# Kernel optimization log

Hardware: AMD Instinct MI355X
Metric: run time of the kernel (lower is better)

Reference implementation:

```python
import jax, jax.numpy as jnp
import numpy as np


def _gru_layer(x, w_ih, w_hh, b_ih, b_hh):
    # x: (T, B, I); w_ih: (3H, I); w_hh: (3H, H). PyTorch gate order: r, z, n.
    H = w_hh.shape[1]
    xg = jnp.einsum('tbi,gi->tbg', x, w_ih) + b_ih  # precompute input gates (T, B, 3H)

    def step(h, xg_t):
        hg = h @ w_hh.T + b_hh
        xr, xz, xn = jnp.split(xg_t, 3, axis=-1)
        hr, hz, hn = jnp.split(hg, 3, axis=-1)
        r = jax.nn.sigmoid(xr + hr)
        z = jax.nn.sigmoid(xz + hz)
        n = jnp.tanh(xn + r * hn)
        h_new = (1.0 - z) * n + z * h
        return h_new, h_new

    h0 = jnp.zeros((x.shape[1], H), dtype=x.dtype)
    _, out = jax.lax.scan(step, h0, xg)
    return out  # (T, B, H)


def setup_inputs() -> dict:
    key = jax.random.key(0)
    ks = jax.random.split(key, 16)
    T, B, V, E, H1, H2 = 1024, 128, 128, 312, 256, 128

    def u(k, shape, fan):
        s = 1.0 / np.sqrt(fan)
        return jax.random.uniform(k, shape, jnp.float32, -s, s)

    return {
        'token': jax.random.randint(ks[0], (T, B), 0, V),
        'emb': jax.random.normal(ks[1], (V, E), jnp.float32),
        'w_ih1': u(ks[2], (3 * H1, E), H1),
        'w_hh1': u(ks[3], (3 * H1, H1), H1),
        'b_ih1': u(ks[4], (3 * H1,), H1),
        'b_hh1': u(ks[5], (3 * H1,), H1),
        'ln_g': jnp.ones((H1,), jnp.float32),
        'ln_b': jnp.zeros((H1,), jnp.float32),
        'w_ih2f': u(ks[6], (3 * H2, H1), H2),
        'w_hh2f': u(ks[7], (3 * H2, H2), H2),
        'b_ih2f': u(ks[8], (3 * H2,), H2),
        'b_hh2f': u(ks[9], (3 * H2,), H2),
        'w_ih2b': u(ks[10], (3 * H2, H1), H2),
        'w_hh2b': u(ks[11], (3 * H2, H2), H2),
        'b_ih2b': u(ks[12], (3 * H2,), H2),
        'b_hh2b': u(ks[13], (3 * H2,), H2),
    }


def reference(token, emb, w_ih1, w_hh1, b_ih1, b_hh1, ln_g, ln_b,
              w_ih2f, w_hh2f, b_ih2f, b_hh2f, w_ih2b, w_hh2b, b_ih2b, b_hh2b):
    LN_EPS = 256.0  # torch.nn.LayerNorm(256, 256): second positional arg is eps (faithful)
    x = emb[token]                                        # (T, B, 312)
    h = _gru_layer(x, w_ih1, w_hh1, b_ih1, b_hh1)         # (T, B, 256)
    mu = jnp.mean(h, axis=-1, keepdims=True)
    var = jnp.mean((h - mu) ** 2, axis=-1, keepdims=True)
    hn = (h - mu) / jnp.sqrt(var + LN_EPS) * ln_g + ln_b  # LayerNorm over last dim
    fwd = _gru_layer(hn, w_ih2f, w_hh2f, b_ih2f, b_hh2f)                 # (T, B, 128)
    bwd = _gru_layer(hn[::-1], w_ih2b, w_hh2b, b_ih2b, b_hh2b)[::-1]     # (T, B, 128)
    return jnp.concatenate([fwd, bwd], axis=-1)           # (T, B, 256)
```

## Files before the change

### kernel.cpp

```cpp
#include <hip/hip_runtime.h>
#include <hip/hip_bf16.h>
#include <stdint.h>

typedef __attribute__((ext_vector_type(8))) short short8;
typedef __attribute__((ext_vector_type(4))) float f32x4;
typedef unsigned long long u64;
typedef unsigned int u32;

__device__ __forceinline__ float bf2f(unsigned short s){
  union { float f; u32 u; } v; v.u = ((u32)s) << 16; return v.f;
}
__device__ __forceinline__ unsigned short f2bf(float f){
  u32 u = __float_as_uint(f);
  u32 r = (u + 0x7fffu + ((u >> 16) & 1u)) >> 16;
  return (unsigned short)r;
}
__device__ __forceinline__ float sigm(float x){ return 1.0f / (1.0f + __expf(-x)); }
__device__ __forceinline__ float tanh_(float x){ return 1.0f - 2.0f/(__expf(2.0f*x) + 1.0f); }
__device__ __forceinline__ u64 pack4(float a, float b, float c, float d){
  return (u64)f2bf(a) | ((u64)f2bf(b)<<16) | ((u64)f2bf(c)<<32) | ((u64)f2bf(d)<<48);
}
__device__ __forceinline__ void gl_lds16(const void* g, void* l){
  __builtin_amdgcn_global_load_lds(
      (const __attribute__((address_space(1))) unsigned int*)g,
      (__attribute__((address_space(3))) unsigned int*)l, 16, 0, 0);
}

__global__ void k_pack(const float* __restrict__ w_hh1,
                       const float* __restrict__ w_ih2f, const float* __restrict__ w_ih2b,
                       const float* __restrict__ w_hh2f, const float* __restrict__ w_hh2b,
                       unsigned short* __restrict__ pack1,
                       unsigned short* __restrict__ pack2,
                       unsigned short* __restrict__ pack3)
{
  int tid = blockIdx.x*256 + threadIdx.x;
  const float* src;
  unsigned short* dst;
  long idx;
  if (tid < 24576){
    int f = tid>>6, l = tid&63;
    int w = f/48, rem = f%48, m = rem>>3, kt = rem&7;
    int g  = ((m>>1)<<8) + (w<<5) + ((m&1)<<4) + (l&15);
    int kb = (kt<<5) + ((l>>4)<<3);
    src = w_hh1 + (size_t)g*256 + kb;
    dst = pack1; idx = tid;
  } else if (tid < 49152){
    int t2 = tid - 24576;
    int f = t2>>6, l = t2&63;
    int w = f/48, rem = f%48, m = rem>>3, kt = rem&7;
    int G  = 96*w + (m<<4) + (l&15);
    int kb = (kt<<5) + ((l>>4)<<3);
    const float* W = (G < 384) ? w_ih2f : w_ih2b;
    src = W + (size_t)(G % 384)*256 + kb;
    dst = pack2; idx = t2;
  } else {
    int t3 = tid - 49152;
    int f = t3>>6, l = t3&63;
    int dir = f/96, r96 = f%96, w = r96/12, r12 = r96%12, m = r12>>2, kt = r12&3;
    int Grow = (m<<7) + (w<<4) + (l&15);
    int kb = (kt<<5) + ((l>>4)<<3);
    src = (dir ? w_hh2b : w_hh2f) + (size_t)Grow*128 + kb;
    dst = pack3; idx = t3;
  }
  u64 lo = (u64)f2bf(src[0]) | ((u64)f2bf(src[1])<<16) | ((u64)f2bf(src[2])<<32) | ((u64)f2bf(src[3])<<48);
  u64 hi = (u64)f2bf(src[4]) | ((u64)f2bf(src[5])<<16) | ((u64)f2bf(src[6])<<32) | ((u64)f2bf(src[7])<<48);
  *(u64*)(dst + (size_t)idx*8)     = lo;
  *(u64*)(dst + (size_t)idx*8 + 4) = hi;
}

__global__ void k_xgv(const float* __restrict__ emb, const float* __restrict__ w_ih1,
                      const float* __restrict__ b_ih1, const float* __restrict__ b_hh1,
                      float* __restrict__ xgV)
{
  int tid = blockIdx.x*256 + threadIdx.x;
  int v = tid / 768, g = tid % 768;
  float s = b_ih1[g] + (g < 512 ? b_hh1[g] : 0.0f);
  const f32x4* e4 = (const f32x4*)(emb   + (size_t)v*312);
  const f32x4* w4 = (const f32x4*)(w_ih1 + (size_t)g*312);
  #pragma unroll 4
  for (int i=0;i<78;i++){
    f32x4 a = e4[i], b = w4[i];
    s += a[0]*b[0] + a[1]*b[1] + a[2]*b[2] + a[3]*b[3];
  }
  xgV[tid] = s;
}

__launch_bounds__(512)
__global__ void k_scan1(const int* __restrict__ token,
                        const float* __restrict__ xgV,
                        const unsigned short* __restrict__ pack1,
                        const float* __restrict__ b_hh1,
                        const float* __restrict__ ln_g, const float* __restrict__ ln_b,
                        unsigned short* __restrict__ hn)
{
  __shared__ __align__(16) char hb[2][8192];
  __shared__ __align__(16) char xgb[2][49152];
  __shared__ __align__(16) float lngb[512];
  __shared__ __align__(16) float bnl[256];
  __shared__ __align__(8)  float2 scr[2][8][16];

  const int tid = threadIdx.x;
  const int w = tid>>6, lane = tid&63, hi = lane>>4, col = lane&15;
  const int b0 = blockIdx.x * 16;

  short8 wf[6][8];
  #pragma unroll
  for (int m=0;m<6;m++)
    #pragma unroll
    for (int kt=0;kt<8;kt++)
      wf[m][kt] = *(const short8*)(pack1 + (size_t)((((w*6+m)<<3)+kt)*64 + lane)*8);

  if (tid < 256) lngb[tid] = ln_g[tid]; else lngb[tid] = ln_b[tid-256];
  if (tid < 256) bnl[tid] = b_hh1[512 + tid];
  for (int i = tid; i < 2048; i += 512) ((u32*)hb[0])[i] = 0;
  f32x4 hr[2]; hr[0] = (f32x4){0,0,0,0}; hr[1] = (f32x4){0,0,0,0};

  auto stage = [&](int tt, int buf){
    int tok = token[tt*128 + b0 + (tid & 15)];
    const char* src = (const char*)xgV + (size_t)tok*3072 + ((tid>>4)<<4);
    char* dst = xgb[buf] + tid*16;
    #pragma unroll
    for (int k=0;k<6;k++)
      gl_lds16(src + k*512, dst + k*8192);
  };
  stage(0, 0);
  __syncthreads();

  for (int t=0; t<1024; t++){
    const int cur = t & 1, nxt = cur ^ 1;
    if (t < 1023) stage(t+1, nxt);

    f32x4 acc[6];
    #pragma unroll
    for (int m=0;m<6;m++) acc[m] = (f32x4){0,0,0,0};
    #pragma unroll
    for (int kt=0;kt<8;kt++){
      short8 hf = *(const short8*)(hb[cur] + ((kt<<2)+hi)*256 + (col<<4));
      #pragma unroll
      for (int m=0;m<6;m++)
        acc[m] = __builtin_amdgcn_mfma_f32_16x16x32_bf16(wf[m][kt], hf, acc[m], 0, 0, 0);
    }

    float s1 = 0.f, s2 = 0.f;
    #pragma unroll
    for (int nt=0;nt<2;nt++){
      const int ub = (w<<5) + (nt<<4) + (hi<<2);
      const char* xb = xgb[cur] + (col<<4);
      f32x4 xr = *(const f32x4*)(xb + (size_t)ub*64);
      f32x4 xz = *(const f32x4*)(xb + (size_t)(256+ub)*64);
      f32x4 xn = *(const f32x4*)(xb + (size_t)(512+ub)*64);
      f32x4 bn4 = *(const f32x4*)(bnl + ub);
      #pragma unroll
      for (int j=0;j<4;j++){
        float r  = sigm(xr[j] + acc[nt][j]);
        float z  = sigm(xz[j] + acc[2+nt][j]);
        float nn = tanh_(xn[j] + r*(acc[4+nt][j] + bn4[j]));
        float h  = nn + z*(hr[nt][j] - nn);
        hr[nt][j] = h;
        s1 += h; s2 += h*h;
      }
      u64 pk = pack4(hr[nt][0], hr[nt][1], hr[nt][2], hr[nt][3]);
      *(u64*)(hb[nxt] + (ub>>3)*256 + (col<<4) + ((hi&1)<<3)) = pk;
    }
    s1 += __shfl_xor(s1, 16); s1 += __shfl_xor(s1, 32);
    s2 += __shfl_xor(s2, 16); s2 += __shfl_xor(s2, 32);
    if (hi == 0){ scr[cur][w][col] = make_float2(s1, s2); }
    __syncthreads();

    float S1 = 0.f, S2 = 0.f;
    #pragma unroll
    for (int ww=0; ww<8; ww++){ float2 v = scr[cur][ww][col]; S1 += v.x; S2 += v.y; }
    float mu  = S1 * (1.0f/256.0f);
    float var = S2 * (1.0f/256.0f) - mu*mu;
    float rs  = rsqrtf(var + 256.0f);
    #pragma unroll
    for (int nt=0;nt<2;nt++){
      const int ub = (w<<5) + (nt<<4) + (hi<<2);
      f32x4 g4 = *(const f32x4*)&lngb[ub];
      f32x4 e4 = *(const f32x4*)&lngb[256+ub];
      u64 pk = pack4((hr[nt][0]-mu)*rs*g4[0] + e4[0],
                     (hr[nt][1]-mu)*rs*g4[1] + e4[1],
                     (hr[nt][2]-mu)*rs*g4[2] + e4[2],
                     (hr[nt][3]-mu)*rs*g4[3] + e4[3]);
      *(u64*)(hn + (size_t)(t*128 + b0 + col)*256 + ub) = pk;
    }
  }
}

__launch_bounds__(512)
__global__ void k_k3(const unsigned short* __restrict__ hn,
                     const unsigned short* __restrict__ pack2,
                     unsigned short* __restrict__ xg2f,
                     unsigned short* __restrict__ xg2b)
{
  const int tid = threadIdx.x;
  const int w = tid>>6, lane = tid&63, hi = lane>>4, col = lane&15;
  short8 wf[6][8];
  #pragma unroll
  for (int m=0;m<6;m++)
    #pragma unroll
    for (int kt=0;kt<8;kt++)
      wf[m][kt] = *(const short8*)(pack2 + (size_t)((((w*6+m)<<3)+kt)*64 + lane)*8);
  const int dir = w >> 2;
  unsigned short* dst = dir ? xg2b : xg2f;

  for (int it=0; it<16; it++){
    int tb0 = blockIdx.x*256 + it*16;
    const unsigned short* hrow = hn + (size_t)(tb0 + col)*256;
    f32x4 acc[6];
    #pragma unroll
    for (int m=0;m<6;m++) acc[m] = (f32x4){0,0,0,0};
    #pragma unroll
    for (int h2=0; h2<2; h2++){
      short8 bf[4];
      #pragma unroll
      for (int i=0;i<4;i++) bf[i] = *(const short8*)(hrow + (((h2<<2)+i)<<5) + (hi<<3));
      #pragma unroll
      for (int i=0;i<4;i++)
        #pragma unroll
        for (int m=0;m<6;m++)
          acc[m] = __builtin_amdgcn_mfma_f32_16x16x32_bf16(wf[m][(h2<<2)+i], bf[i], acc[m], 0, 0, 0);
    }
    #pragma unroll
    for (int m=0;m<6;m++){
      int Gl = 96*w + (m<<4) + (hi<<2) - dir*384;
      u64 pk = pack4(acc[m][0], acc[m][1], acc[m][2], acc[m][3]);
      *(u64*)(dst + (size_t)(tb0 + col)*384 + Gl) = pk;
    }
  }
}

__launch_bounds__(512)
__global__ void k_scan2(const unsigned short* __restrict__ xg2f,
                        const unsigned short* __restrict__ xg2b,
                        const unsigned short* __restrict__ pack3,
                        const float* __restrict__ b_ih2f, const float* __restrict__ b_hh2f,
                        const float* __restrict__ b_ih2b, const float* __restrict__ b_hh2b,
                        float* __restrict__ out)
{
  __shared__ __align__(16) char hb[2][4096];
  const int tid = threadIdx.x;
  const int w = tid>>6, lane = tid&63, hi = lane>>4, col = lane&15;
  const int blk = blockIdx.x;
  const int dir = blk >> 3;
  const int b0  = (blk & 7) * 16;
  const unsigned short* xg = dir ? xg2b : xg2f;
  const float* bi = dir ? b_ih2b : b_ih2f;
  const float* bh = dir ? b_hh2b : b_hh2f;

  short8 wf[3][4];
  #pragma unroll
  for (int m=0;m<3;m++)
    #pragma unroll
    for (int kt=0;kt<4;kt++)
      wf[m][kt] = *(const short8*)(pack3 + (size_t)(((dir*96 + w*12 + (m<<2) + kt))*64 + lane)*8);

  const int u = (w<<4) + (hi<<2);
  f32x4 bir = *(const f32x4*)(bi + u),        bhr = *(const f32x4*)(bh + u);
  f32x4 biz = *(const f32x4*)(bi + 128 + u),  bhz = *(const f32x4*)(bh + 128 + u);
  f32x4 bin = *(const f32x4*)(bi + 256 + u),  bhn = *(const f32x4*)(bh + 256 + u);
  f32x4 bcr = bir + bhr, bcz = biz + bhz;

  for (int i = tid; i < 1024; i += 512) ((u32*)hb[0])[i] = 0;
  f32x4 hcur = (f32x4){0,0,0,0};

  int te0 = dir ? 1023 : 0;
  const unsigned short* p0 = xg + (size_t)(te0*128 + b0 + col)*384;
  u64 xr_n = *(const u64*)(p0 + u);
  u64 xz_n = *(const u64*)(p0 + 128 + u);
  u64 xn_n = *(const u64*)(p0 + 256 + u);
  __syncthreads();

  for (int t=0; t<1024; t++){
    const int cur = t & 1, nxt = cur ^ 1;
    u64 xr = xr_n, xz = xz_n, xn = xn_n;
    if (t < 1023){
      int te1 = dir ? (1022 - t) : (t + 1);
      const unsigned short* p = xg + (size_t)(te1*128 + b0 + col)*384;
      xr_n = *(const u64*)(p + u);
      xz_n = *(const u64*)(p + 128 + u);
      xn_n = *(const u64*)(p + 256 + u);
    }
    f32x4 acc[3];
    #pragma unroll
    for (int m=0;m<3;m++) acc[m] = (f32x4){0,0,0,0};
    #pragma unroll
    for (int kt=0;kt<4;kt++){
      short8 hf = *(const short8*)(hb[cur] + ((kt<<2)+hi)*256 + (col<<4));
      #pragma unroll
      for (int m=0;m<3;m++)
        acc[m] = __builtin_amdgcn_mfma_f32_16x16x32_bf16(wf[m][kt], hf, acc[m], 0, 0, 0);
    }
    const int te = dir ? (1023 - t) : t;
    f32x4 hnew;
    #pragma unroll
    for (int j=0;j<4;j++){
      float r  = sigm(bf2f((unsigned short)(xr >> (16*j))) + bcr[j] + acc[0][j]);
      float z  = sigm(bf2f((unsigned short)(xz >> (16*j))) + bcz[j] + acc[1][j]);
      float nn = tanh_(bf2f((unsigned short)(xn >> (16*j))) + bin[j] + r*(acc[2][j] + bhn[j]));
      hnew[j] = nn + z*(hcur[j] - nn);
    }
    hcur = hnew;
    *(f32x4*)(out + (size_t)(te*128 + b0 + col)*256 + dir*128 + u) = hnew;
    u64 pk = pack4(hnew[0], hnew[1], hnew[2], hnew[3]);
    *(u64*)(hb[nxt] + ((u>>3))*256 + (col<<4) + ((hi&1)<<3)) = pk;
    __syncthreads();
  }
}

extern "C" void kernel_launch(void* const* d_in, const int* in_sizes, int n_in,
                              void* d_out, int out_size, void* d_ws, size_t ws_size,
                              hipStream_t stream)
{
  (void)in_sizes; (void)n_in; (void)out_size; (void)ws_size;
  const int*   token  = (const int*)  d_in[0];
  const float* emb    = (const float*)d_in[1];
  const float* w_ih1  = (const float*)d_in[2];
  const float* w_hh1  = (const float*)d_in[3];
  const float* b_ih1  = (const float*)d_in[4];
  const float* b_hh1  = (const float*)d_in[5];
  const float* ln_g   = (const float*)d_in[6];
  const float* ln_b   = (const float*)d_in[7];
  const float* w_ih2f = (const float*)d_in[8];
  const float* w_hh2f = (const float*)d_in[9];
  const float* b_ih2f = (const float*)d_in[10];
  const float* b_hh2f = (const float*)d_in[11];
  const float* w_ih2b = (const float*)d_in[12];
  const float* w_hh2b = (const float*)d_in[13];
  const float* b_ih2b = (const float*)d_in[14];
  const float* b_hh2b = (const float*)d_in[15];
  float* out = (float*)d_out;

  char* ws = (char*)d_ws;
  unsigned short* hn    = (unsigned short*)(ws);
  unsigned short* xg2f  = (unsigned short*)(ws + 67108864);
  unsigned short* xg2b  = (unsigned short*)(ws + 167772160);
  float*          xgV   = (float*)(ws + 167772160);
  unsigned short* pack1 = (unsigned short*)(ws + 268632064);
  unsigned short* pack2 = (unsigned short*)(ws + 269025280);
  unsigned short* pack3 = (unsigned short*)(ws + 269418496);

  hipLaunchKernelGGL(k_pack,  dim3(240), dim3(256), 0, stream,
                     w_hh1, w_ih2f, w_ih2b, w_hh2f, w_hh2b, pack1, pack2, pack3);
  hipLaunchKernelGGL(k_xgv,   dim3(384), dim3(256), 0, stream,
                     emb, w_ih1, b_ih1, b_hh1, xgV);
  hipLaunchKernelGGL(k_scan1, dim3(8),   dim3(512), 0, stream,
                     token, xgV, pack1, b_hh1, ln_g, ln_b, hn);
  hipLaunchKernelGGL(k_k3,    dim3(512), dim3(512), 0, stream,
                     hn, pack2, xg2f, xg2b);
  hipLaunchKernelGGL(k_scan2, dim3(16),  dim3(512), 0, stream,
                     xg2f, xg2b, pack3, b_ih2f, b_hh2f, b_ih2b, b_hh2b, out);
}
```

Measured before the change: 6.083 ms.

## Double waves per block in layer-1 scan and input-gate GEMM

```diff
diff --git a/kernel.cpp b/kernel.cpp
--- a/kernel.cpp
+++ b/kernel.cpp
@@ -39,16 +39,16 @@
   long idx;
   if (tid < 24576){
     int f = tid>>6, l = tid&63;
-    int w = f/48, rem = f%48, m = rem>>3, kt = rem&7;
-    int g  = ((m>>1)<<8) + (w<<5) + ((m&1)<<4) + (l&15);
+    int w = f/24, rem = f%24, m = rem>>3, kt = rem&7;
+    int g  = (m<<8) + (w<<4) + (l&15);
     int kb = (kt<<5) + ((l>>4)<<3);
     src = w_hh1 + (size_t)g*256 + kb;
     dst = pack1; idx = tid;
   } else if (tid < 49152){
     int t2 = tid - 24576;
     int f = t2>>6, l = t2&63;
-    int w = f/48, rem = f%48, m = rem>>3, kt = rem&7;
-    int G  = 96*w + (m<<4) + (l&15);
+    int w = f/24, rem = f%24, m = rem>>3, kt = rem&7;
+    int G  = 48*w + (m<<4) + (l&15);
     int kb = (kt<<5) + ((l>>4)<<3);
     const float* W = (G < 384) ? w_ih2f : w_ih2b;
     src = W + (size_t)(G % 384)*256 + kb;
@@ -85,7 +85,7 @@
   xgV[tid] = s;
 }
 
-__launch_bounds__(512)
+__launch_bounds__(1024)
 __global__ void k_scan1(const int* __restrict__ token,
                         const float* __restrict__ xgV,
                         const unsigned short* __restrict__ pack1,
@@ -97,31 +97,32 @@
   __shared__ __align__(16) char xgb[2][49152];
   __shared__ __align__(16) float lngb[512];
   __shared__ __align__(16) float bnl[256];
-  __shared__ __align__(8)  float2 scr[2][8][16];
+  __shared__ __align__(8)  float2 scr[2][16][16];
 
   const int tid = threadIdx.x;
   const int w = tid>>6, lane = tid&63, hi = lane>>4, col = lane&15;
   const int b0 = blockIdx.x * 16;
-
-  short8 wf[6][8];
+  const int ub = (w<<4) + (hi<<2);
+
+  short8 wf[3][8];
   #pragma unroll
-  for (int m=0;m<6;m++)
+  for (int m=0;m<3;m++)
     #pragma unroll
     for (int kt=0;kt<8;kt++)
-      wf[m][kt] = *(const short8*)(pack1 + (size_t)((((w*6+m)<<3)+kt)*64 + lane)*8);
-
-  if (tid < 256) lngb[tid] = ln_g[tid]; else lngb[tid] = ln_b[tid-256];
-  if (tid < 256) bnl[tid] = b_hh1[512 + tid];
-  for (int i = tid; i < 2048; i += 512) ((u32*)hb[0])[i] = 0;
-  f32x4 hr[2]; hr[0] = (f32x4){0,0,0,0}; hr[1] = (f32x4){0,0,0,0};
+      wf[m][kt] = *(const short8*)(pack1 + (size_t)((((w*3+m)<<3)+kt)*64 + lane)*8);
+
+  if (tid < 512){ if (tid < 256) lngb[tid] = ln_g[tid]; else lngb[tid] = ln_b[tid-256]; }
+  if (tid >= 512 && tid < 768) bnl[tid-512] = b_hh1[512 + (tid-512)];
+  for (int i = tid; i < 2048; i += 1024) ((u32*)hb[0])[i] = 0;
+  f32x4 hr = (f32x4){0,0,0,0};
 
   auto stage = [&](int tt, int buf){
     int tok = token[tt*128 + b0 + (tid & 15)];
     const char* src = (const char*)xgV + (size_t)tok*3072 + ((tid>>4)<<4);
     char* dst = xgb[buf] + tid*16;
     #pragma unroll
-    for (int k=0;k<6;k++)
-      gl_lds16(src + k*512, dst + k*8192);
+    for (int k=0;k<3;k++)
+      gl_lds16(src + k*1024, dst + k*16384);
   };
   stage(0, 0);
   __syncthreads();
@@ -130,36 +131,34 @@
     const int cur = t & 1, nxt = cur ^ 1;
     if (t < 1023) stage(t+1, nxt);
 
-    f32x4 acc[6];
-    #pragma unroll
-    for (int m=0;m<6;m++) acc[m] = (f32x4){0,0,0,0};
+    f32x4 acc[3];
+    #pragma unroll
+    for (int m=0;m<3;m++) acc[m] = (f32x4){0,0,0,0};
     #pragma unroll
     for (int kt=0;kt<8;kt++){
       short8 hf = *(const short8*)(hb[cur] + ((kt<<2)+hi)*256 + (col<<4));
       #pragma unroll
-      for (int m=0;m<6;m++)
+      for (int m=0;m<3;m++)
         acc[m] = __builtin_amdgcn_mfma_f32_16x16x32_bf16(wf[m][kt], hf, acc[m], 0, 0, 0);
     }
 
     float s1 = 0.f, s2 = 0.f;
-    #pragma unroll
-    for (int nt=0;nt<2;nt++){
-      const int ub = (w<<5) + (nt<<4) + (hi<<2);
+    {
       const char* xb = xgb[cur] + (col<<4);
-      f32x4 xr = *(const f32x4*)(xb + (size_t)ub*64);
-      f32x4 xz = *(const f32x4*)(xb + (size_t)(256+ub)*64);
-      f32x4 xn = *(const f32x4*)(xb + (size_t)(512+ub)*64);
+      f32x4 xr = *(const f32x4*)(xb + ((size_t)ub<<6));
+      f32x4 xz = *(const f32x4*)(xb + ((size_t)(256+ub)<<6));
+      f32x4 xn = *(const f32x4*)(xb + ((size_t)(512+ub)<<6));
       f32x4 bn4 = *(const f32x4*)(bnl + ub);
       #pragma unroll
       for (int j=0;j<4;j++){
-        float r  = sigm(xr[j] + acc[nt][j]);
-        float z  = sigm(xz[j] + acc[2+nt][j]);
-        float nn = tanh_(xn[j] + r*(acc[4+nt][j] + bn4[j]));
-        float h  = nn + z*(hr[nt][j] - nn);
-        hr[nt][j] = h;
+        float r  = sigm(xr[j] + acc[0][j]);
+        float z  = sigm(xz[j] + acc[1][j]);
+        float nn = tanh_(xn[j] + r*(acc[2][j] + bn4[j]));
+        float h  = nn + z*(hr[j] - nn);
+        hr[j] = h;
         s1 += h; s2 += h*h;
       }
-      u64 pk = pack4(hr[nt][0], hr[nt][1], hr[nt][2], hr[nt][3]);
+      u64 pk = pack4(hr[0], hr[1], hr[2], hr[3]);
       *(u64*)(hb[nxt] + (ub>>3)*256 + (col<<4) + ((hi&1)<<3)) = pk;
     }
     s1 += __shfl_xor(s1, 16); s1 += __shfl_xor(s1, 32);
@@ -169,25 +168,23 @@
 
     float S1 = 0.f, S2 = 0.f;
     #pragma unroll
-    for (int ww=0; ww<8; ww++){ float2 v = scr[cur][ww][col]; S1 += v.x; S2 += v.y; }
+    for (int ww=0; ww<16; ww++){ float2 v = scr[cur][ww][col]; S1 += v.x; S2 += v.y; }
     float mu  = S1 * (1.0f/256.0f);
     float var = S2 * (1.0f/256.0f) - mu*mu;
     float rs  = rsqrtf(var + 256.0f);
-    #pragma unroll
-    for (int nt=0;nt<2;nt++){
-      const int ub = (w<<5) + (nt<<4) + (hi<<2);
+    {
       f32x4 g4 = *(const f32x4*)&lngb[ub];
       f32x4 e4 = *(const f32x4*)&lngb[256+ub];
-      u64 pk = pack4((hr[nt][0]-mu)*rs*g4[0] + e4[0],
-                     (hr[nt][1]-mu)*rs*g4[1] + e4[1],
-                     (hr[nt][2]-mu)*rs*g4[2] + e4[2],
-                     (hr[nt][3]-mu)*rs*g4[3] + e4[3]);
+      u64 pk = pack4((hr[0]-mu)*rs*g4[0] + e4[0],
+                     (hr[1]-mu)*rs*g4[1] + e4[1],
+                     (hr[2]-mu)*rs*g4[2] + e4[2],
+                     (hr[3]-mu)*rs*g4[3] + e4[3]);
       *(u64*)(hn + (size_t)(t*128 + b0 + col)*256 + ub) = pk;
     }
   }
 }
 
-__launch_bounds__(512)
+__launch_bounds__(1024)
 __global__ void k_k3(const unsigned short* __restrict__ hn,
                      const unsigned short* __restrict__ pack2,
                      unsigned short* __restrict__ xg2f,
@@ -195,35 +192,31 @@
 {
   const int tid = threadIdx.x;
   const int w = tid>>6, lane = tid&63, hi = lane>>4, col = lane&15;
-  short8 wf[6][8];
+  short8 wf[3][8];
   #pragma unroll
-  for (int m=0;m<6;m++)
+  for (int m=0;m<3;m++)
     #pragma unroll
     for (int kt=0;kt<8;kt++)
-      wf[m][kt] = *(const short8*)(pack2 + (size_t)((((w*6+m)<<3)+kt)*64 + lane)*8);
-  const int dir = w >> 2;
+      wf[m][kt] = *(const short8*)(pack2 + (size_t)((((w*3+m)<<3)+kt)*64 + lane)*8);
+  const int dir = w >> 3;
   unsigned short* dst = dir ? xg2b : xg2f;
 
   for (int it=0; it<16; it++){
     int tb0 = blockIdx.x*256 + it*16;
     const unsigned short* hrow = hn + (size_t)(tb0 + col)*256;
-    f32x4 acc[6];
-    #pragma unroll
-    for (int m=0;m<6;m++) acc[m] = (f32x4){0,0,0,0};
-    #pragma unroll
-    for (int h2=0; h2<2; h2++){
-      short8 bf[4];
+    f32x4 acc[3];
+    #pragma unroll
+    for (int m=0;m<3;m++) acc[m] = (f32x4){0,0,0,0};
+    #pragma unroll
+    for (int kt=0;kt<8;kt++){
+      short8 hf = *(const short8*)(hrow + (kt<<5) + (hi<<3));
       #pragma unroll
-      for (int i=0;i<4;i++) bf[i] = *(const short8*)(hrow + (((h2<<2)+i)<<5) + (hi<<3));
-      #pragma unroll
-      for (int i=0;i<4;i++)
-        #pragma unroll
-        for (int m=0;m<6;m++)
-          acc[m] = __builtin_amdgcn_mfma_f32_16x16x32_bf16(wf[m][(h2<<2)+i], bf[i], acc[m], 0, 0, 0);
-    }
-    #pragma unroll
-    for (int m=0;m<6;m++){
-      int Gl = 96*w + (m<<4) + (hi<<2) - dir*384;
+      for (int m=0;m<3;m++)
+        acc[m] = __builtin_amdgcn_mfma_f32_16x16x32_bf16(wf[m][kt], hf, acc[m], 0, 0, 0);
+    }
+    #pragma unroll
+    for (int m=0;m<3;m++){
+      int Gl = 48*w + (m<<4) + (hi<<2) - dir*384;
       u64 pk = pack4(acc[m][0], acc[m][1], acc[m][2], acc[m][3]);
       *(u64*)(dst + (size_t)(tb0 + col)*384 + Gl) = pk;
     }
@@ -344,9 +337,9 @@
                      w_hh1, w_ih2f, w_ih2b, w_hh2f, w_hh2b, pack1, pack2, pack3);
   hipLaunchKernelGGL(k_xgv,   dim3(384), dim3(256), 0, stream,
                      emb, w_ih1, b_ih1, b_hh1, xgV);
-  hipLaunchKernelGGL(k_scan1, dim3(8),   dim3(512), 0, stream,
+  hipLaunchKernelGGL(k_scan1, dim3(8),   dim3(1024), 0, stream,
                      token, xgV, pack1, b_hh1, ln_g, ln_b, hn);
-  hipLaunchKernelGGL(k_k3,    dim3(512), dim3(512), 0, stream,
+  hipLaunchKernelGGL(k_k3,    dim3(512), dim3(1024), 0, stream,
                      hn, pack2, xg2f, xg2b);
   hipLaunchKernelGGL(k_scan2, dim3(16),  dim3(512), 0, stream,
                      xg2f, xg2b, pack3, b_ih2f, b_hh2f, b_ih2b, b_hh2b, out);
```

Result: slower. 7.422 ms (+22.0%).

## Split layer-1 GRU scan across paired workgroups with global-memory flag exchange

Applied to the files above, without the earlier changes.

```diff
diff --git a/kernel.cpp b/kernel.cpp
--- a/kernel.cpp
+++ b/kernel.cpp
@@ -39,16 +39,16 @@
   long idx;
   if (tid < 24576){
     int f = tid>>6, l = tid&63;
-    int w = f/48, rem = f%48, m = rem>>3, kt = rem&7;
-    int g  = ((m>>1)<<8) + (w<<5) + ((m&1)<<4) + (l&15);
+    int s = f/48, rem = f%48, m = rem>>3, kt = rem&7;
+    int g  = ((m>>1)<<8) + (s<<5) + ((m&1)<<4) + (l&15);
     int kb = (kt<<5) + ((l>>4)<<3);
     src = w_hh1 + (size_t)g*256 + kb;
     dst = pack1; idx = tid;
   } else if (tid < 49152){
     int t2 = tid - 24576;
     int f = t2>>6, l = t2&63;
-    int w = f/48, rem = f%48, m = rem>>3, kt = rem&7;
-    int G  = 96*w + (m<<4) + (l&15);
+    int s = f/48, rem = f%48, m = rem>>3, kt = rem&7;
+    int G  = 96*s + (m<<4) + (l&15);
     int kb = (kt<<5) + ((l>>4)<<3);
     const float* W = (G < 384) ? w_ih2f : w_ih2b;
     src = W + (size_t)(G % 384)*256 + kb;
@@ -70,9 +70,10 @@
 
 __global__ void k_xgv(const float* __restrict__ emb, const float* __restrict__ w_ih1,
                       const float* __restrict__ b_ih1, const float* __restrict__ b_hh1,
-                      float* __restrict__ xgV)
+                      float* __restrict__ xgV, u32* __restrict__ flg)
 {
   int tid = blockIdx.x*256 + threadIdx.x;
+  if (tid < 16) flg[tid] = 0;
   int v = tid / 768, g = tid % 768;
   float s = b_ih1[g] + (g < 512 ? b_hh1[g] : 0.0f);
   const f32x4* e4 = (const f32x4*)(emb   + (size_t)v*312);
@@ -85,43 +86,51 @@
   xgV[tid] = s;
 }
 
-__launch_bounds__(512)
+__launch_bounds__(256)
 __global__ void k_scan1(const int* __restrict__ token,
                         const float* __restrict__ xgV,
                         const unsigned short* __restrict__ pack1,
                         const float* __restrict__ b_hh1,
                         const float* __restrict__ ln_g, const float* __restrict__ ln_b,
-                        unsigned short* __restrict__ hn)
+                        unsigned short* __restrict__ hn,
+                        u64* __restrict__ hx, u64* __restrict__ px,
+                        u32* __restrict__ flg)
 {
   __shared__ __align__(16) char hb[2][8192];
-  __shared__ __align__(16) char xgb[2][49152];
-  __shared__ __align__(16) float lngb[512];
-  __shared__ __align__(16) float bnl[256];
-  __shared__ __align__(8)  float2 scr[2][8][16];
+  __shared__ __align__(16) char lxg[2][24576];
+  __shared__ __align__(16) float lng[128];
+  __shared__ __align__(16) float lnb[128];
+  __shared__ __align__(16) float bnl[128];
+  __shared__ __align__(8)  float2 scr[4][16];
 
   const int tid = threadIdx.x;
   const int w = tid>>6, lane = tid&63, hi = lane>>4, col = lane&15;
-  const int b0 = blockIdx.x * 16;
+  const int g = blockIdx.x >> 1, p = blockIdx.x & 1;
+  const int s = p*4 + w;
+  const int b0 = g*16;
+  const int myf = g*2 + p, otf = g*2 + (1-p);
 
   short8 wf[6][8];
   #pragma unroll
   for (int m=0;m<6;m++)
     #pragma unroll
     for (int kt=0;kt<8;kt++)
-      wf[m][kt] = *(const short8*)(pack1 + (size_t)((((w*6+m)<<3)+kt)*64 + lane)*8);
-
-  if (tid < 256) lngb[tid] = ln_g[tid]; else lngb[tid] = ln_b[tid-256];
-  if (tid < 256) bnl[tid] = b_hh1[512 + tid];
-  for (int i = tid; i < 2048; i += 512) ((u32*)hb[0])[i] = 0;
+      wf[m][kt] = *(const short8*)(pack1 + (size_t)((s*48 + m*8 + kt)*64 + lane)*8);
+
+  if (tid < 128){ lng[tid] = ln_g[128*p + tid]; bnl[tid] = b_hh1[512 + 128*p + tid]; }
+  else          { lnb[tid-128] = ln_b[128*p + tid-128]; }
+  for (int i = tid; i < 2048; i += 256) ((u32*)hb[0])[i] = 0;
   f32x4 hr[2]; hr[0] = (f32x4){0,0,0,0}; hr[1] = (f32x4){0,0,0,0};
 
   auto stage = [&](int tt, int buf){
     int tok = token[tt*128 + b0 + (tid & 15)];
-    const char* src = (const char*)xgV + (size_t)tok*3072 + ((tid>>4)<<4);
-    char* dst = xgb[buf] + tid*16;
-    #pragma unroll
-    for (int k=0;k<6;k++)
-      gl_lds16(src + k*512, dst + k*8192);
+    const char* srcb = (const char*)xgV + (size_t)tok*3072 + p*512;
+    char* dst = lxg[buf] + (tid>>4)*256 + (tid&15)*16;
+    #pragma unroll
+    for (int k=0;k<6;k++){
+      int c = (tid>>4) + 16*k;
+      gl_lds16(srcb + (c>>5)*1024 + (c&31)*16, dst + k*4096);
+    }
   };
   stage(0, 0);
   __syncthreads();
@@ -142,14 +151,15 @@
     }
 
     float s1 = 0.f, s2 = 0.f;
+    u64 pkv[2];
     #pragma unroll
     for (int nt=0;nt<2;nt++){
-      const int ub = (w<<5) + (nt<<4) + (hi<<2);
-      const char* xb = xgb[cur] + (col<<4);
-      f32x4 xr = *(const f32x4*)(xb + (size_t)ub*64);
-      f32x4 xz = *(const f32x4*)(xb + (size_t)(256+ub)*64);
-      f32x4 xn = *(const f32x4*)(xb + (size_t)(512+ub)*64);
-      f32x4 bn4 = *(const f32x4*)(bnl + ub);
+      const int lu = (w<<5) + (nt<<4) + (hi<<2);
+      const char* xb = lxg[cur] + (col<<4);
+      f32x4 xr  = *(const f32x4*)(xb + (size_t)(lu>>2)*256);
+      f32x4 xz  = *(const f32x4*)(xb + (size_t)((lu>>2)+32)*256);
+      f32x4 xn  = *(const f32x4*)(xb + (size_t)((lu>>2)+64)*256);
+      f32x4 bn4 = *(const f32x4*)(bnl + lu);
       #pragma unroll
       for (int j=0;j<4;j++){
         float r  = sigm(xr[j] + acc[nt][j]);
@@ -159,35 +169,74 @@
         hr[nt][j] = h;
         s1 += h; s2 += h*h;
       }
-      u64 pk = pack4(hr[nt][0], hr[nt][1], hr[nt][2], hr[nt][3]);
-      *(u64*)(hb[nxt] + (ub>>3)*256 + (col<<4) + ((hi&1)<<3)) = pk;
+      pkv[nt] = pack4(hr[nt][0], hr[nt][1], hr[nt][2], hr[nt][3]);
+    }
+    {
+      size_t hxb = ((((size_t)cur*8 + g)*2 + p)*16 + col)*32;
+      __hip_atomic_store(hx + hxb + ((w<<3)     + hi), pkv[0],
+                         __ATOMIC_RELAXED, __HIP_MEMORY_SCOPE_AGENT);
+      __hip_atomic_store(hx + hxb + ((w<<3) + 4 + hi), pkv[1],
+                         __ATOMIC_RELAXED, __HIP_MEMORY_SCOPE_AGENT);
+    }
+    #pragma unroll
+    for (int nt=0;nt<2;nt++){
+      int u = 128*p + (w<<5) + (nt<<4) + (hi<<2);
+      *(u64*)(hb[nxt] + (u>>3)*256 + (col<<4) + ((hi&1)<<3)) = pkv[nt];
     }
     s1 += __shfl_xor(s1, 16); s1 += __shfl_xor(s1, 32);
     s2 += __shfl_xor(s2, 16); s2 += __shfl_xor(s2, 32);
-    if (hi == 0){ scr[cur][w][col] = make_float2(s1, s2); }
+    if (hi == 0) scr[w][col] = make_float2(s1, s2);
     __syncthreads();
 
-    float S1 = 0.f, S2 = 0.f;
-    #pragma unroll
-    for (int ww=0; ww<8; ww++){ float2 v = scr[cur][ww][col]; S1 += v.x; S2 += v.y; }
+    float S1h = 0.f, S2h = 0.f;
+    #pragma unroll
+    for (int ww=0; ww<4; ww++){ float2 v = scr[ww][col]; S1h += v.x; S2h += v.y; }
+    if (tid < 16){
+      union{ float f[2]; u64 u; } pv; pv.f[0] = S1h; pv.f[1] = S2h;
+      __hip_atomic_store(px + (((size_t)cur*8 + g)*2 + p)*16 + col, pv.u,
+                         __ATOMIC_RELAXED, __HIP_MEMORY_SCOPE_AGENT);
+    }
+    asm volatile("s_waitcnt vmcnt(0)" ::: "memory");
+    if (lane == 0)
+      __hip_atomic_fetch_add(&flg[myf], 1u, __ATOMIC_RELAXED, __HIP_MEMORY_SCOPE_AGENT);
+    const u32 need = 4u*(u32)(t+1);
+    while (__hip_atomic_load(&flg[otf], __ATOMIC_RELAXED, __HIP_MEMORY_SCOPE_AGENT) < need)
+      __builtin_amdgcn_s_sleep(1);
+
+    size_t oxb = ((((size_t)cur*8 + g)*2 + (1-p))*16 + col)*32;
+    u64 oh0 = __hip_atomic_load(hx + oxb + ((w<<3)     + hi),
+                                __ATOMIC_RELAXED, __HIP_MEMORY_SCOPE_AGENT);
+    u64 oh1 = __hip_atomic_load(hx + oxb + ((w<<3) + 4 + hi),
+                                __ATOMIC_RELAXED, __HIP_MEMORY_SCOPE_AGENT);
+    u64 pxo = __hip_atomic_load(px + (((size_t)cur*8 + g)*2 + (1-p))*16 + col,
+                                __ATOMIC_RELAXED, __HIP_MEMORY_SCOPE_AGENT);
+    {
+      int u0 = 128*(1-p) + (w<<5) + (hi<<2);
+      *(u64*)(hb[nxt] + (u0>>3)*256 + (col<<4) + ((hi&1)<<3)) = oh0;
+      int u1 = u0 + 16;
+      *(u64*)(hb[nxt] + (u1>>3)*256 + (col<<4) + ((hi&1)<<3)) = oh1;
+    }
+    union{ u64 u; float f[2]; } pv2; pv2.u = pxo;
+    float S1 = S1h + pv2.f[0], S2 = S2h + pv2.f[1];
     float mu  = S1 * (1.0f/256.0f);
     float var = S2 * (1.0f/256.0f) - mu*mu;
     float rs  = rsqrtf(var + 256.0f);
     #pragma unroll
     for (int nt=0;nt<2;nt++){
-      const int ub = (w<<5) + (nt<<4) + (hi<<2);
-      f32x4 g4 = *(const f32x4*)&lngb[ub];
-      f32x4 e4 = *(const f32x4*)&lngb[256+ub];
+      const int lu = (w<<5) + (nt<<4) + (hi<<2);
+      f32x4 g4 = *(const f32x4*)(lng + lu);
+      f32x4 e4 = *(const f32x4*)(lnb + lu);
       u64 pk = pack4((hr[nt][0]-mu)*rs*g4[0] + e4[0],
                      (hr[nt][1]-mu)*rs*g4[1] + e4[1],
                      (hr[nt][2]-mu)*rs*g4[2] + e4[2],
                      (hr[nt][3]-mu)*rs*g4[3] + e4[3]);
-      *(u64*)(hn + (size_t)(t*128 + b0 + col)*256 + ub) = pk;
-    }
+      *(u64*)(hn + (size_t)(t*128 + b0 + col)*256 + 128*p + lu) = pk;
+    }
+    __syncthreads();
   }
 }
 
-__launch_bounds__(512)
+__launch_bounds__(256)
 __global__ void k_k3(const unsigned short* __restrict__ hn,
                      const unsigned short* __restrict__ pack2,
                      unsigned short* __restrict__ xg2f,
@@ -195,35 +244,32 @@
 {
   const int tid = threadIdx.x;
   const int w = tid>>6, lane = tid&63, hi = lane>>4, col = lane&15;
+  const int dir = blockIdx.x & 1;
+  const int s = dir*4 + w;
   short8 wf[6][8];
   #pragma unroll
   for (int m=0;m<6;m++)
     #pragma unroll
     for (int kt=0;kt<8;kt++)
-      wf[m][kt] = *(const short8*)(pack2 + (size_t)((((w*6+m)<<3)+kt)*64 + lane)*8);
-  const int dir = w >> 2;
+      wf[m][kt] = *(const short8*)(pack2 + (size_t)((s*48 + m*8 + kt)*64 + lane)*8);
   unsigned short* dst = dir ? xg2b : xg2f;
 
-  for (int it=0; it<16; it++){
-    int tb0 = blockIdx.x*256 + it*16;
+  for (int it=0; it<32; it++){
+    int tb0 = (blockIdx.x>>1)*512 + it*16;
     const unsigned short* hrow = hn + (size_t)(tb0 + col)*256;
     f32x4 acc[6];
     #pragma unroll
     for (int m=0;m<6;m++) acc[m] = (f32x4){0,0,0,0};
     #pragma unroll
-    for (int h2=0; h2<2; h2++){
-      short8 bf[4];
+    for (int kt=0;kt<8;kt++){
+      short8 hf = *(const short8*)(hrow + (kt<<5) + (hi<<3));
       #pragma unroll
-      for (int i=0;i<4;i++) bf[i] = *(const short8*)(hrow + (((h2<<2)+i)<<5) + (hi<<3));
-      #pragma unroll
-      for (int i=0;i<4;i++)
-        #pragma unroll
-        for (int m=0;m<6;m++)
-          acc[m] = __builtin_amdgcn_mfma_f32_16x16x32_bf16(wf[m][(h2<<2)+i], bf[i], acc[m], 0, 0, 0);
+      for (int m=0;m<6;m++)
+        acc[m] = __builtin_amdgcn_mfma_f32_16x16x32_bf16(wf[m][kt], hf, acc[m], 0, 0, 0);
     }
     #pragma unroll
     for (int m=0;m<6;m++){
-      int Gl = 96*w + (m<<4) + (hi<<2) - dir*384;
+      int Gl = 96*w + (m<<4) + (hi<<2);
       u64 pk = pack4(acc[m][0], acc[m][1], acc[m][2], acc[m][3]);
       *(u64*)(dst + (size_t)(tb0 + col)*384 + Gl) = pk;
     }
@@ -339,14 +385,17 @@
   unsigned short* pack1 = (unsigned short*)(ws + 268632064);
   unsigned short* pack2 = (unsigned short*)(ws + 269025280);
   unsigned short* pack3 = (unsigned short*)(ws + 269418496);
+  u64*            hx    = (u64*)          (ws + 269615104);
+  u64*            px    = (u64*)          (ws + 269746176);
+  u32*            flg   = (u32*)          (ws + 269750272);
 
   hipLaunchKernelGGL(k_pack,  dim3(240), dim3(256), 0, stream,
                      w_hh1, w_ih2f, w_ih2b, w_hh2f, w_hh2b, pack1, pack2, pack3);
   hipLaunchKernelGGL(k_xgv,   dim3(384), dim3(256), 0, stream,
-                     emb, w_ih1, b_ih1, b_hh1, xgV);
-  hipLaunchKernelGGL(k_scan1, dim3(8),   dim3(512), 0, stream,
-                     token, xgV, pack1, b_hh1, ln_g, ln_b, hn);
-  hipLaunchKernelGGL(k_k3,    dim3(512), dim3(512), 0, stream,
+                     emb, w_ih1, b_ih1, b_hh1, xgV, flg);
+  hipLaunchKernelGGL(k_scan1, dim3(16),  dim3(256), 0, stream,
+                     token, xgV, pack1, b_hh1, ln_g, ln_b, hn, hx, px, flg);
+  hipLaunchKernelGGL(k_k3,    dim3(512), dim3(256), 0, stream,
                      hn, pack2, xg2f, xg2b);
   hipLaunchKernelGGL(k_scan2, dim3(16),  dim3(512), 0, stream,
                      xg2f, xg2b, pack3, b_ih2f, b_hh2f, b_ih2b, b_hh2b, out);
```

Result: slower. 7.474 ms (+22.9%).

## Halve wave count in layer-1 scan and input-gate GEMM, doubling per-wave work

Applied to the files above, without the earlier changes.

```diff
diff --git a/kernel.cpp b/kernel.cpp
--- a/kernel.cpp
+++ b/kernel.cpp
@@ -39,16 +39,16 @@
   long idx;
   if (tid < 24576){
     int f = tid>>6, l = tid&63;
-    int w = f/48, rem = f%48, m = rem>>3, kt = rem&7;
-    int g  = ((m>>1)<<8) + (w<<5) + ((m&1)<<4) + (l&15);
+    int w = f/96, rem = f%96, kt = rem&7, ms = rem>>3, G = ms>>2, s = ms&3;
+    int g  = (G<<8) + (w<<6) + (s<<4) + (l&15);
     int kb = (kt<<5) + ((l>>4)<<3);
     src = w_hh1 + (size_t)g*256 + kb;
     dst = pack1; idx = tid;
   } else if (tid < 49152){
     int t2 = tid - 24576;
     int f = t2>>6, l = t2&63;
-    int w = f/48, rem = f%48, m = rem>>3, kt = rem&7;
-    int G  = 96*w + (m<<4) + (l&15);
+    int s = f/48, rem = f%48, m = rem>>3, kt = rem&7;
+    int G  = 96*s + (m<<4) + (l&15);
     int kb = (kt<<5) + ((l>>4)<<3);
     const float* W = (G < 384) ? w_ih2f : w_ih2b;
     src = W + (size_t)(G % 384)*256 + kb;
@@ -85,7 +85,7 @@
   xgV[tid] = s;
 }
 
-__launch_bounds__(512)
+__launch_bounds__(256)
 __global__ void k_scan1(const int* __restrict__ token,
                         const float* __restrict__ xgV,
                         const unsigned short* __restrict__ pack1,
@@ -97,31 +97,31 @@
   __shared__ __align__(16) char xgb[2][49152];
   __shared__ __align__(16) float lngb[512];
   __shared__ __align__(16) float bnl[256];
-  __shared__ __align__(8)  float2 scr[2][8][16];
+  __shared__ __align__(8)  float2 scr[2][4][16];
 
   const int tid = threadIdx.x;
   const int w = tid>>6, lane = tid&63, hi = lane>>4, col = lane&15;
   const int b0 = blockIdx.x * 16;
 
-  short8 wf[6][8];
+  short8 wf[12][8];
   #pragma unroll
-  for (int m=0;m<6;m++)
-    #pragma unroll
-    for (int kt=0;kt<8;kt++)
-      wf[m][kt] = *(const short8*)(pack1 + (size_t)((((w*6+m)<<3)+kt)*64 + lane)*8);
-
-  if (tid < 256) lngb[tid] = ln_g[tid]; else lngb[tid] = ln_b[tid-256];
-  if (tid < 256) bnl[tid] = b_hh1[512 + tid];
-  for (int i = tid; i < 2048; i += 512) ((u32*)hb[0])[i] = 0;
-  f32x4 hr[2]; hr[0] = (f32x4){0,0,0,0}; hr[1] = (f32x4){0,0,0,0};
+  for (int ms=0; ms<12; ms++)
+    #pragma unroll
+    for (int kt=0; kt<8; kt++)
+      wf[ms][kt] = *(const short8*)(pack1 + (size_t)(((w*12+ms)*8+kt)*64 + lane)*8);
+
+  for (int i=tid; i<512; i+=256) lngb[i] = (i<256) ? ln_g[i] : ln_b[i-256];
+  bnl[tid] = b_hh1[512 + tid];
+  for (int i=tid; i<2048; i+=256) ((u32*)hb[0])[i] = 0;
+  f32x4 hr0={0,0,0,0}, hr1={0,0,0,0}, hr2={0,0,0,0}, hr3={0,0,0,0};
 
   auto stage = [&](int tt, int buf){
     int tok = token[tt*128 + b0 + (tid & 15)];
     const char* src = (const char*)xgV + (size_t)tok*3072 + ((tid>>4)<<4);
-    char* dst = xgb[buf] + tid*16;
-    #pragma unroll
-    for (int k=0;k<6;k++)
-      gl_lds16(src + k*512, dst + k*8192);
+    char* dst = xgb[buf] + (tid>>4)*256 + (tid&15)*16;
+    #pragma unroll
+    for (int k=0;k<12;k++)
+      gl_lds16(src + k*256, dst + k*4096);
   };
   stage(0, 0);
   __syncthreads();
@@ -130,64 +130,66 @@
     const int cur = t & 1, nxt = cur ^ 1;
     if (t < 1023) stage(t+1, nxt);
 
-    f32x4 acc[6];
-    #pragma unroll
-    for (int m=0;m<6;m++) acc[m] = (f32x4){0,0,0,0};
+    f32x4 acc[12];
+    #pragma unroll
+    for (int ms=0;ms<12;ms++) acc[ms] = (f32x4){0,0,0,0};
     #pragma unroll
     for (int kt=0;kt<8;kt++){
       short8 hf = *(const short8*)(hb[cur] + ((kt<<2)+hi)*256 + (col<<4));
       #pragma unroll
-      for (int m=0;m<6;m++)
-        acc[m] = __builtin_amdgcn_mfma_f32_16x16x32_bf16(wf[m][kt], hf, acc[m], 0, 0, 0);
+      for (int ms=0;ms<12;ms++)
+        acc[ms] = __builtin_amdgcn_mfma_f32_16x16x32_bf16(wf[ms][kt], hf, acc[ms], 0, 0, 0);
     }
 
     float s1 = 0.f, s2 = 0.f;
     #pragma unroll
-    for (int nt=0;nt<2;nt++){
-      const int ub = (w<<5) + (nt<<4) + (hi<<2);
+    for (int s=0;s<4;s++){
+      const int ub = (w<<6) + (s<<4) + (hi<<2);
       const char* xb = xgb[cur] + (col<<4);
-      f32x4 xr = *(const f32x4*)(xb + (size_t)ub*64);
-      f32x4 xz = *(const f32x4*)(xb + (size_t)(256+ub)*64);
-      f32x4 xn = *(const f32x4*)(xb + (size_t)(512+ub)*64);
+      f32x4 xr  = *(const f32x4*)(xb + (size_t)(ub>>2)*256);
+      f32x4 xz  = *(const f32x4*)(xb + (size_t)((ub>>2)+64)*256);
+      f32x4 xn  = *(const f32x4*)(xb + (size_t)((ub>>2)+128)*256);
       f32x4 bn4 = *(const f32x4*)(bnl + ub);
+      f32x4 h = (s==0)?hr0:(s==1)?hr1:(s==2)?hr2:hr3;
       #pragma unroll
       for (int j=0;j<4;j++){
-        float r  = sigm(xr[j] + acc[nt][j]);
-        float z  = sigm(xz[j] + acc[2+nt][j]);
-        float nn = tanh_(xn[j] + r*(acc[4+nt][j] + bn4[j]));
-        float h  = nn + z*(hr[nt][j] - nn);
-        hr[nt][j] = h;
-        s1 += h; s2 += h*h;
+        float r  = sigm(xr[j] + acc[s][j]);
+        float z  = sigm(xz[j] + acc[4+s][j]);
+        float nn = tanh_(xn[j] + r*(acc[8+s][j] + bn4[j]));
+        float hh = nn + z*(h[j] - nn);
+        h[j] = hh; s1 += hh; s2 += hh*hh;
       }
-      u64 pk = pack4(hr[nt][0], hr[nt][1], hr[nt][2], hr[nt][3]);
-      *(u64*)(hb[nxt] + (ub>>3)*256 + (col<<4) + ((hi&1)<<3)) = pk;
+      if (s==0) hr0=h; else if (s==1) hr1=h; else if (s==2) hr2=h; else hr3=h;
+      *(u64*)(hb[nxt] + (ub>>3)*256 + (col<<4) + ((hi&1)<<3)) =
+          pack4(h[0],h[1],h[2],h[3]);
     }
     s1 += __shfl_xor(s1, 16); s1 += __shfl_xor(s1, 32);
     s2 += __shfl_xor(s2, 16); s2 += __shfl_xor(s2, 32);
-    if (hi == 0){ scr[cur][w][col] = make_float2(s1, s2); }
+    if (hi == 0) scr[cur][w][col] = make_float2(s1, s2);
     __syncthreads();
 
     float S1 = 0.f, S2 = 0.f;
     #pragma unroll
-    for (int ww=0; ww<8; ww++){ float2 v = scr[cur][ww][col]; S1 += v.x; S2 += v.y; }
+    for (int ww=0; ww<4; ww++){ float2 v = scr[cur][ww][col]; S1 += v.x; S2 += v.y; }
     float mu  = S1 * (1.0f/256.0f);
     float var = S2 * (1.0f/256.0f) - mu*mu;
     float rs  = rsqrtf(var + 256.0f);
     #pragma unroll
-    for (int nt=0;nt<2;nt++){
-      const int ub = (w<<5) + (nt<<4) + (hi<<2);
+    for (int s=0;s<4;s++){
+      const int ub = (w<<6) + (s<<4) + (hi<<2);
       f32x4 g4 = *(const f32x4*)&lngb[ub];
       f32x4 e4 = *(const f32x4*)&lngb[256+ub];
-      u64 pk = pack4((hr[nt][0]-mu)*rs*g4[0] + e4[0],
-                     (hr[nt][1]-mu)*rs*g4[1] + e4[1],
-                     (hr[nt][2]-mu)*rs*g4[2] + e4[2],
-                     (hr[nt][3]-mu)*rs*g4[3] + e4[3]);
+      f32x4 h = (s==0)?hr0:(s==1)?hr1:(s==2)?hr2:hr3;
+      u64 pk = pack4((h[0]-mu)*rs*g4[0] + e4[0],
+                     (h[1]-mu)*rs*g4[1] + e4[1],
+                     (h[2]-mu)*rs*g4[2] + e4[2],
+                     (h[3]-mu)*rs*g4[3] + e4[3]);
       *(u64*)(hn + (size_t)(t*128 + b0 + col)*256 + ub) = pk;
     }
   }
 }
 
-__launch_bounds__(512)
+__launch_bounds__(256)
 __global__ void k_k3(const unsigned short* __restrict__ hn,
                      const unsigned short* __restrict__ pack2,
                      unsigned short* __restrict__ xg2f,
@@ -195,35 +197,32 @@
 {
   const int tid = threadIdx.x;
   const int w = tid>>6, lane = tid&63, hi = lane>>4, col = lane&15;
+  const int dir = blockIdx.x & 1;
+  const int s = dir*4 + w;
   short8 wf[6][8];
   #pragma unroll
   for (int m=0;m<6;m++)
     #pragma unroll
     for (int kt=0;kt<8;kt++)
-      wf[m][kt] = *(const short8*)(pack2 + (size_t)((((w*6+m)<<3)+kt)*64 + lane)*8);
-  const int dir = w >> 2;
+      wf[m][kt] = *(const short8*)(pack2 + (size_t)((s*48 + m*8 + kt)*64 + lane)*8);
   unsigned short* dst = dir ? xg2b : xg2f;
 
-  for (int it=0; it<16; it++){
-    int tb0 = blockIdx.x*256 + it*16;
+  for (int it=0; it<32; it++){
+    int tb0 = (blockIdx.x>>1)*512 + it*16;
     const unsigned short* hrow = hn + (size_t)(tb0 + col)*256;
     f32x4 acc[6];
     #pragma unroll
     for (int m=0;m<6;m++) acc[m] = (f32x4){0,0,0,0};
     #pragma unroll
-    for (int h2=0; h2<2; h2++){
-      short8 bf[4];
+    for (int kt=0;kt<8;kt++){
+      short8 hf = *(const short8*)(hrow + (kt<<5) + (hi<<3));
       #pragma unroll
-      for (int i=0;i<4;i++) bf[i] = *(const short8*)(hrow + (((h2<<2)+i)<<5) + (hi<<3));
-      #pragma unroll
-      for (int i=0;i<4;i++)
-        #pragma unroll
-        for (int m=0;m<6;m++)
-          acc[m] = __builtin_amdgcn_mfma_f32_16x16x32_bf16(wf[m][(h2<<2)+i], bf[i], acc[m], 0, 0, 0);
+      for (int m=0;m<6;m++)
+        acc[m] = __builtin_amdgcn_mfma_f32_16x16x32_bf16(wf[m][kt], hf, acc[m], 0, 0, 0);
     }
     #pragma unroll
     for (int m=0;m<6;m++){
-      int Gl = 96*w + (m<<4) + (hi<<2) - dir*384;
+      int Gl = 96*w + (m<<4) + (hi<<2);
       u64 pk = pack4(acc[m][0], acc[m][1], acc[m][2], acc[m][3]);
       *(u64*)(dst + (size_t)(tb0 + col)*384 + Gl) = pk;
     }
@@ -344,9 +343,9 @@
                      w_hh1, w_ih2f, w_ih2b, w_hh2f, w_hh2b, pack1, pack2, pack3);
   hipLaunchKernelGGL(k_xgv,   dim3(384), dim3(256), 0, stream,
                      emb, w_ih1, b_ih1, b_hh1, xgV);
-  hipLaunchKernelGGL(k_scan1, dim3(8),   dim3(512), 0, stream,
+  hipLaunchKernelGGL(k_scan1, dim3(8),   dim3(256), 0, stream,
                      token, xgV, pack1, b_hh1, ln_g, ln_b, hn);
-  hipLaunchKernelGGL(k_k3,    dim3(512), dim3(512), 0, stream,
+  hipLaunchKernelGGL(k_k3,    dim3(512), dim3(256), 0, stream,
                      hn, pack2, xg2f, xg2b);
   hipLaunchKernelGGL(k_scan2, dim3(16),  dim3(512), 0, stream,
                      xg2f, xg2b, pack3, b_ih2f, b_hh2f, b_ih2b, b_hh2b, out);
```

Result: slower. 7.426 ms (+22.1%).
